# Kernel tuning notes

Measured on AMD Instinct MI355X. Metric: run time of the kernel, lower is better.

## Reference

```python
import jax, jax.numpy as jnp
import numpy as np

D = 1024  # in_features == latent_dim
EPS = 1e-5


def _layernorm(x, g, b):
    mu = jnp.mean(x, axis=-1, keepdims=True)
    var = jnp.mean(jnp.square(x - mu), axis=-1, keepdims=True)
    return (x - mu) * jax.lax.rsqrt(var + EPS) * g + b


def setup_inputs() -> dict:
    key = jax.random.key(0)
    ks = jax.random.split(key, 8)
    s = 1.0 / np.sqrt(D)
    return {
        "x": jax.random.normal(ks[0], (4, 4096, D), dtype=jnp.float32),
        "w_qkv": jax.random.uniform(ks[1], (3 * D, D), jnp.float32, -s, s),
        "w_o": jax.random.uniform(ks[2], (D, D), jnp.float32, -s, s),
        "w1": jax.random.uniform(ks[3], (D, D), jnp.float32, -s, s),
        "b1": jax.random.uniform(ks[4], (D,), jnp.float32, -s, s),
        "w2": jax.random.uniform(ks[5], (D, D), jnp.float32, -s, s),
        "b2": jax.random.uniform(ks[6], (D,), jnp.float32, -s, s),
        "ln1_g": jnp.ones((D,), jnp.float32),
        "ln1_b": jnp.zeros((D,), jnp.float32),
        "ln2_g": jnp.ones((D,), jnp.float32),
        "ln2_b": jnp.zeros((D,), jnp.float32),
    }


def reference(x, w_qkv, w_o, w1, b1, w2, b2, ln1_g, ln1_b, ln2_g, ln2_b):
    B, S, _ = x.shape
    scale = 1.0 / np.sqrt(D * 1)  # 1/sqrt(latent_dim * n_heads), n_heads=1
    qkv = jnp.einsum("bsd,ed->bse", x, w_qkv)            # [B,S,3D]
    qkv = qkv.reshape(B, S, 1, 3 * D).transpose(0, 2, 1, 3)  # [B,1,S,3D]
    q, k, v = jnp.split(qkv, 3, axis=-1)                  # each [B,1,S,D]
    logits = jnp.einsum("bhid,bhjd->bhij", q, k) * scale  # [B,1,S,S]
    # Faithful quirk: softmax over the HEAD axis (dim=1). With 1 head this
    # yields an all-ones attention matrix.
    attn = jax.nn.softmax(logits, axis=1)
    vals = jnp.einsum("bhij,bhjd->bhid", attn, v)         # [B,1,S,D]
    vals = vals.transpose(0, 2, 1, 3).reshape(B, S, D)
    attn_out = jnp.einsum("bsd,ed->bse", vals, w_o)
    # squeeze(-2) is a no-op for S>1
    x = _layernorm(x + attn_out, ln1_g, ln1_b)
    h = jax.nn.gelu(jnp.einsum("bsd,ed->bse", x, w1) + b1, approximate=False)
    mlp_out = jnp.einsum("bsd,ed->bse", h, w2) + b2
    return _layernorm(x + mlp_out, ln2_g, ln2_b)
```

## Files before the change

### kernel.cpp

```cpp
#include <hip/hip_runtime.h>
#include <hip/hip_bf16.h>

typedef __hip_bfloat16 bf16;
typedef __attribute__((ext_vector_type(8))) short short8;
typedef __attribute__((ext_vector_type(4))) float f32x4;

#define DDIM 1024
#define SEQ  4096
#define NB   4
#define MTOT (NB*SEQ)

static __device__ __forceinline__ unsigned short f2bf(float f) {
    __hip_bfloat16 h = __float2bfloat16(f);
    unsigned short u; __builtin_memcpy(&u, &h, 2); return u;
}
static __device__ __forceinline__ float bf2f(unsigned short u) {
    __hip_bfloat16 h; __builtin_memcpy(&h, &u, 2); return __bfloat162float(h);
}

__global__ __launch_bounds__(256) void prep_kernel(
    const float* __restrict__ w1, const float* __restrict__ w2,
    unsigned short* __restrict__ w1b, unsigned short* __restrict__ w2b,
    const float* __restrict__ x, float* __restrict__ partial)
{
    int bid = blockIdx.x;
    if (bid < 1024) {
        size_t idx = ((size_t)bid*256 + threadIdx.x) * 4;
        float4 a = *(const float4*)(w1 + idx);
        ushort4 o; o.x=f2bf(a.x); o.y=f2bf(a.y); o.z=f2bf(a.z); o.w=f2bf(a.w);
        *(ushort4*)(w1b + idx) = o;
        float4 b = *(const float4*)(w2 + idx);
        o.x=f2bf(b.x); o.y=f2bf(b.y); o.z=f2bf(b.z); o.w=f2bf(b.w);
        *(ushort4*)(w2b + idx) = o;
    } else {
        int idx = bid - 1024;
        int dx = idx & 3, b = (idx >> 2) & 3, sl = idx >> 4;
        int d  = dx*256 + threadIdx.x;
        const float* p = x + ((size_t)b*SEQ + (size_t)sl*128)*DDIM + d;
        float s = 0.f;
        #pragma unroll 4
        for (int i = 0; i < 128; ++i) s += p[(size_t)i*DDIM];
        partial[((size_t)sl*NB + b)*DDIM + d] = s;
    }
}

__global__ __launch_bounds__(256) void colsum_reduce_kernel(
    const float* __restrict__ partial, float* __restrict__ xsum)
{
    int d = blockIdx.x*256 + threadIdx.x;
    int b = blockIdx.y;
    float s = 0.f;
    #pragma unroll
    for (int sl = 0; sl < 32; ++sl) s += partial[((size_t)sl*NB + b)*DDIM + d];
    xsum[b*DDIM + d] = s;
}

__global__ __launch_bounds__(256) void matvec_kernel(
    const float* __restrict__ W, const float* __restrict__ vin, float* __restrict__ vout)
{
    int b = blockIdx.y;
    int g = threadIdx.x >> 4;
    int t = threadIdx.x & 15;
    int e = blockIdx.x*16 + g;
    const float* w = W + (size_t)e*DDIM;
    const float* v = vin + b*DDIM;
    float s = 0.f;
    for (int k = t; k < DDIM; k += 16) s += w[k]*v[k];
    #pragma unroll
    for (int o = 8; o; o >>= 1) s += __shfl_down(s, o, 16);
    if (t == 0) vout[b*DDIM + e] = s;
}

__global__ __launch_bounds__(256) void ln1_kernel(
    const float* __restrict__ x, const float* __restrict__ avec,
    const float* __restrict__ g1, const float* __restrict__ b1,
    unsigned short* __restrict__ x1b)
{
    int row = blockIdx.x;
    int b   = row >> 12;
    int tid = threadIdx.x;
    const float4* xr = (const float4*)(x + (size_t)row*DDIM);
    const float4* av = (const float4*)(avec + (size_t)b*DDIM);
    float4 xv = xr[tid], a4 = av[tid];
    float y0 = xv.x+a4.x, y1 = xv.y+a4.y, y2 = xv.z+a4.z, y3 = xv.w+a4.w;
    float s  = y0+y1+y2+y3;
    float ss = y0*y0+y1*y1+y2*y2+y3*y3;
    #pragma unroll
    for (int o = 32; o; o >>= 1) { s += __shfl_down(s,o,64); ss += __shfl_down(ss,o,64); }
    __shared__ float red[8];
    if ((tid&63) == 0) { red[tid>>6] = s; red[4+(tid>>6)] = ss; }
    __syncthreads();
    float St = red[0]+red[1]+red[2]+red[3];
    float Sq = red[4]+red[5]+red[6]+red[7];
    float mu = St*(1.0f/DDIM);
    float rs = rsqrtf(Sq*(1.0f/DDIM) - mu*mu + 1e-5f);
    float4 g4 = ((const float4*)g1)[tid];
    float4 bb = ((const float4*)b1)[tid];
    ushort4 o;
    o.x = f2bf((y0-mu)*rs*g4.x + bb.x);
    o.y = f2bf((y1-mu)*rs*g4.y + bb.y);
    o.z = f2bf((y2-mu)*rs*g4.z + bb.z);
    o.w = f2bf((y3-mu)*rs*g4.w + bb.w);
    *(ushort4*)(x1b + (size_t)row*DDIM + tid*4) = o;
}

__global__ __launch_bounds__(256, 2) void gemm1_kernel(
    const bf16* __restrict__ A, const bf16* __restrict__ Bw,
    const float* __restrict__ bias, unsigned short* __restrict__ outb)
{
    constexpr int K = 1024, N = 1024, BK = 64, NT = K / BK;
    __shared__ __align__(16) bf16 lds[2][2][128*BK];
    const int tid  = threadIdx.x;
    const int wave = tid >> 6, lane = tid & 63;

    int bid = blockIdx.x;
    int swz = (bid & 7) * 128 + (bid >> 3);
    const size_t bm = (size_t)(swz >> 3) * 128;
    const size_t bn = (size_t)(swz & 7) * 128;

    const int wm = wave >> 1;
    const int wn = wave & 1;

    const int srow = tid >> 3;
    const int skel = (((tid & 7) ^ ((tid >> 3) & 7)) << 3);

    const int fr = lane & 15;
    const int fs = lane >> 4;
    int foff[2];
    #pragma unroll
    for (int ks = 0; ks < 2; ++ks)
        foff[ks] = fr*128 + (((ks*4 + fs) ^ (fr & 7)) << 4);

    f32x4 acc[4][4] = {};
    const bf16* Ab = A  + bm * K;
    const bf16* Bb = Bw + bn * K;

    auto stage = [&](int b, int kt) {
        #pragma unroll
        for (int mat = 0; mat < 2; ++mat) {
            const bf16* src = (mat == 0 ? Ab : Bb);
            #pragma unroll
            for (int g = 0; g < 4; ++g) {
                int row = g*32 + srow;
                const bf16* gp = src + (size_t)row * K + kt*BK + skel;
                __builtin_amdgcn_global_load_lds(
                    (const __attribute__((address_space(1))) void*)gp,
                    (__attribute__((address_space(3))) void*)
                        ((char*)&lds[b][mat][0] + g*4096 + wave*1024),
                    16, 0, 0);
            }
        }
    };

    stage(0, 0);

    #pragma unroll 2
    for (int t = 0; t < NT; ++t) {
        const int cur = t & 1;
        if (t < NT-1) {
            stage(cur ^ 1, t + 1);
            asm volatile("s_waitcnt vmcnt(8)" ::: "memory");
        } else {
            asm volatile("s_waitcnt vmcnt(0)" ::: "memory");
        }
        __builtin_amdgcn_s_barrier();

        const char* LA = (const char*)&lds[cur][0][0] + wm*8192;
        const char* LB = (const char*)&lds[cur][1][0] + wn*8192;
        #pragma unroll
        for (int ks = 0; ks < 2; ++ks) {
            short8 af[4], bfr[4];
            #pragma unroll
            for (int m = 0; m < 4; ++m) af[m]  = *(const short8*)(LA + m*2048 + foff[ks]);
            #pragma unroll
            for (int n = 0; n < 4; ++n) bfr[n] = *(const short8*)(LB + n*2048 + foff[ks]);
            __builtin_amdgcn_s_setprio(1);
            #pragma unroll
            for (int m = 0; m < 4; ++m)
                #pragma unroll
                for (int n = 0; n < 4; ++n)
                    acc[m][n] = __builtin_amdgcn_mfma_f32_16x16x32_bf16(
                        af[m], bfr[n], acc[m][n], 0, 0, 0);
            __builtin_amdgcn_s_setprio(0);
        }
        __builtin_amdgcn_s_barrier();
    }

    #pragma unroll
    for (int n = 0; n < 4; ++n) {
        size_t col = bn + wn*64 + n*16 + fr;
        float bv = bias[col];
        #pragma unroll
        for (int m = 0; m < 4; ++m) {
            #pragma unroll
            for (int r = 0; r < 4; ++r) {
                size_t row = bm + wm*64 + m*16 + fs*4 + r;
                float v = acc[m][n][r] + bv;
                float ge = 0.5f*v*(1.0f + erff(v*0.70710678118f));
                outb[row*(size_t)N + col] = f2bf(ge);
            }
        }
    }
}

__global__ __launch_bounds__(256, 2) void gemm2_kernel(
    const bf16* __restrict__ A, const bf16* __restrict__ Bw,
    const float* __restrict__ bias, unsigned short* __restrict__ xy,
    float2* __restrict__ part)
{
    constexpr int K = 1024, N = 1024, BK = 64, NT = K / BK;
    __shared__ __align__(16) bf16 lds[2][2][128*BK];
    const int tid  = threadIdx.x;
    const int wave = tid >> 6, lane = tid & 63;

    int bid = blockIdx.x;
    int swz = (bid & 7) * 128 + (bid >> 3);
    const size_t bm = (size_t)(swz >> 3) * 128;
    const size_t bn = (size_t)(swz & 7) * 128;

    const int wm = wave >> 1;
    const int wn = wave & 1;

    const int srow = tid >> 3;
    const int skel = (((tid & 7) ^ ((tid >> 3) & 7)) << 3);

    const int fr = lane & 15;
    const int fs = lane >> 4;
    int foff[2];
    #pragma unroll
    for (int ks = 0; ks < 2; ++ks)
        foff[ks] = fr*128 + (((ks*4 + fs) ^ (fr & 7)) << 4);

    f32x4 acc[4][4] = {};
    const bf16* Ab = A  + bm * K;
    const bf16* Bb = Bw + bn * K;

    auto stage = [&](int b, int kt) {
        #pragma unroll
        for (int mat = 0; mat < 2; ++mat) {
            const bf16* src = (mat == 0 ? Ab : Bb);
            #pragma unroll
            for (int g = 0; g < 4; ++g) {
                int row = g*32 + srow;
                const bf16* gp = src + (size_t)row * K + kt*BK + skel;
                __builtin_amdgcn_global_load_lds(
                    (const __attribute__((address_space(1))) void*)gp,
                    (__attribute__((address_space(3))) void*)
                        ((char*)&lds[b][mat][0] + g*4096 + wave*1024),
                    16, 0, 0);
            }
        }
    };

    stage(0, 0);

    #pragma unroll 2
    for (int t = 0; t < NT; ++t) {
        const int cur = t & 1;
        if (t < NT-1) {
            stage(cur ^ 1, t + 1);
            asm volatile("s_waitcnt vmcnt(8)" ::: "memory");
        } else {
            asm volatile("s_waitcnt vmcnt(0)" ::: "memory");
        }
        __builtin_amdgcn_s_barrier();

        const char* LA = (const char*)&lds[cur][0][0] + wm*8192;
        const char* LB = (const char*)&lds[cur][1][0] + wn*8192;
        #pragma unroll
        for (int ks = 0; ks < 2; ++ks) {
            short8 af[4], bfr[4];
            #pragma unroll
            for (int m = 0; m < 4; ++m) af[m]  = *(const short8*)(LA + m*2048 + foff[ks]);
            #pragma unroll
            for (int n = 0; n < 4; ++n) bfr[n] = *(const short8*)(LB + n*2048 + foff[ks]);
            __builtin_amdgcn_s_setprio(1);
            #pragma unroll
            for (int m = 0; m < 4; ++m)
                #pragma unroll
                for (int n = 0; n < 4; ++n)
                    acc[m][n] = __builtin_amdgcn_mfma_f32_16x16x32_bf16(
                        af[m], bfr[n], acc[m][n], 0, 0, 0);
            __builtin_amdgcn_s_setprio(0);
        }
        __builtin_amdgcn_s_barrier();
    }

    float vs[4][4] = {}, vq[4][4] = {};
    #pragma unroll
    for (int n = 0; n < 4; ++n) {
        size_t col = bn + wn*64 + n*16 + fr;
        float bv = bias[col];
        #pragma unroll
        for (int m = 0; m < 4; ++m) {
            #pragma unroll
            for (int r = 0; r < 4; ++r) {
                size_t row = bm + wm*64 + m*16 + fs*4 + r;
                size_t idx = row*(size_t)N + col;
                float v = acc[m][n][r] + bv + bf2f(xy[idx]);
                unsigned short qb = f2bf(v);
                xy[idx] = qb;
                float vv = bf2f(qb);
                vs[m][r] += vv;
                vq[m][r] += vv*vv;
            }
        }
    }
    #pragma unroll
    for (int o = 1; o < 16; o <<= 1) {
        #pragma unroll
        for (int m = 0; m < 4; ++m)
            #pragma unroll
            for (int r = 0; r < 4; ++r) {
                vs[m][r] += __shfl_xor(vs[m][r], o);
                vq[m][r] += __shfl_xor(vq[m][r], o);
            }
    }
    float* lred = (float*)&lds[0][0][0];
    if (fr == 0) {
        #pragma unroll
        for (int m = 0; m < 4; ++m)
            #pragma unroll
            for (int r = 0; r < 4; ++r) {
                int rl = wm*64 + m*16 + fs*4 + r;
                lred[(wn*128 + rl)*2]     = vs[m][r];
                lred[(wn*128 + rl)*2 + 1] = vq[m][r];
            }
    }
    __syncthreads();
    if (tid < 128) {
        float s  = lred[tid*2]       + lred[(128 + tid)*2];
        float sq = lred[tid*2 + 1]   + lred[(128 + tid)*2 + 1];
        part[(bm + tid)*8 + (bn >> 7)] = make_float2(s, sq);
    }
}

__global__ __launch_bounds__(256) void ln2_apply_kernel(
    const unsigned short* __restrict__ yb, const float2* __restrict__ part,
    const float* __restrict__ g2, const float* __restrict__ b2,
    float* __restrict__ out)
{
    int row = blockIdx.x;
    int tid = threadIdx.x;
    float s = 0.f, sq = 0.f;
    #pragma unroll
    for (int i = 0; i < 8; ++i) {
        float2 p = part[(size_t)row*8 + i];
        s += p.x; sq += p.y;
    }
    float mu = s * (1.0f/DDIM);
    float rs = rsqrtf(sq * (1.0f/DDIM) - mu*mu + 1e-5f);
    ushort4 yv = *(const ushort4*)(yb + (size_t)row*DDIM + tid*4);
    float4 g4 = ((const float4*)g2)[tid];
    float4 bb = ((const float4*)b2)[tid];
    float4 o;
    o.x = (bf2f(yv.x) - mu)*rs*g4.x + bb.x;
    o.y = (bf2f(yv.y) - mu)*rs*g4.y + bb.y;
    o.z = (bf2f(yv.z) - mu)*rs*g4.z + bb.z;
    o.w = (bf2f(yv.w) - mu)*rs*g4.w + bb.w;
    ((float4*)(out + (size_t)row*DDIM))[tid] = o;
}

extern "C" void kernel_launch(void* const* d_in, const int* in_sizes, int n_in,
                              void* d_out, int out_size, void* d_ws, size_t ws_size,
                              hipStream_t stream)
{
    const float* x     = (const float*)d_in[0];
    const float* w_qkv = (const float*)d_in[1];
    const float* w_o   = (const float*)d_in[2];
    const float* w1    = (const float*)d_in[3];
    const float* b1    = (const float*)d_in[4];
    const float* w2    = (const float*)d_in[5];
    const float* b2    = (const float*)d_in[6];
    const float* ln1g  = (const float*)d_in[7];
    const float* ln1b  = (const float*)d_in[8];
    const float* ln2g  = (const float*)d_in[9];
    const float* ln2b  = (const float*)d_in[10];
    float* out = (float*)d_out;
    char* ws = (char*)d_ws;

    unsigned short* x1b = (unsigned short*)(ws);
    unsigned short* hb  = (unsigned short*)(ws + 33554432);
    unsigned short* w1b = (unsigned short*)(ws + 67108864);
    unsigned short* w2b = (unsigned short*)(ws + 69206016);
    float* partial = (float*)(ws + 71303168);
    float* xsum    = (float*)(ws + 71827456);
    float* tvec    = (float*)(ws + 71843840);
    float* avec    = (float*)(ws + 71860224);
    float2* lnpart = (float2*)(ws + 67108864);

    prep_kernel<<<dim3(1536), 256, 0, stream>>>(w1, w2, w1b, w2b, x, partial);
    colsum_reduce_kernel<<<dim3(4, NB), 256, 0, stream>>>(partial, xsum);
    matvec_kernel<<<dim3(64, NB), 256, 0, stream>>>(w_qkv + (size_t)2*DDIM*DDIM, xsum, tvec);
    matvec_kernel<<<dim3(64, NB), 256, 0, stream>>>(w_o, tvec, avec);
    ln1_kernel<<<dim3(MTOT), 256, 0, stream>>>(x, avec, ln1g, ln1b, x1b);
    gemm1_kernel<<<dim3(1024), 256, 0, stream>>>(
        (const bf16*)x1b, (const bf16*)w1b, b1, hb);
    gemm2_kernel<<<dim3(1024), 256, 0, stream>>>(
        (const bf16*)hb, (const bf16*)w2b, b2, x1b, lnpart);
    ln2_apply_kernel<<<dim3(MTOT), 256, 0, stream>>>(x1b, lnpart, ln2g, ln2b, out);
}
```

Measured before the change: 171.3 us.

## Fuse LN2 apply into gemm2 via last-block atomic counter; merge colsum into matvec

Removes the separate ln2_apply launch. Each gemm2 block bumps a per-row-block atomic counter, and the last of the 8 column blocks normalizes and writes the 128 output rows. The column-sum reduce kernel is also folded into the first matvec, which rebuilds the summed vector in LDS in every block. The trade-off is a serialized 128-row tail done by one block per row group, redundant partial-sum reads across the 64 matvec blocks, and a dependence on threadfence ordering for correctness.

```diff
diff --git a/kernel.cpp b/kernel.cpp
--- a/kernel.cpp
+++ b/kernel.cpp
@@ -21,9 +21,11 @@
 __global__ __launch_bounds__(256) void prep_kernel(
     const float* __restrict__ w1, const float* __restrict__ w2,
     unsigned short* __restrict__ w1b, unsigned short* __restrict__ w2b,
-    const float* __restrict__ x, float* __restrict__ partial)
+    const float* __restrict__ x, float* __restrict__ partial,
+    int* __restrict__ cnt)
 {
     int bid = blockIdx.x;
+    if (bid == 0 && threadIdx.x < 128) cnt[threadIdx.x] = 0;
     if (bid < 1024) {
         size_t idx = ((size_t)bid*256 + threadIdx.x) * 4;
         float4 a = *(const float4*)(w1 + idx);
@@ -44,15 +46,30 @@
     }
 }
 
-__global__ __launch_bounds__(256) void colsum_reduce_kernel(
-    const float* __restrict__ partial, float* __restrict__ xsum)
-{
-    int d = blockIdx.x*256 + threadIdx.x;
+__global__ __launch_bounds__(256) void matvec1_kernel(
+    const float* __restrict__ W, const float* __restrict__ partial,
+    float* __restrict__ vout)
+{
     int b = blockIdx.y;
+    __shared__ float vloc[DDIM];
+    #pragma unroll
+    for (int j = 0; j < 4; ++j) {
+        int d = j*256 + threadIdx.x;
+        float s = 0.f;
+        #pragma unroll
+        for (int sl = 0; sl < 32; ++sl) s += partial[((size_t)sl*NB + b)*DDIM + d];
+        vloc[d] = s;
+    }
+    __syncthreads();
+    int g = threadIdx.x >> 4;
+    int t = threadIdx.x & 15;
+    int e = blockIdx.x*16 + g;
+    const float* w = W + (size_t)e*DDIM;
     float s = 0.f;
-    #pragma unroll
-    for (int sl = 0; sl < 32; ++sl) s += partial[((size_t)sl*NB + b)*DDIM + d];
-    xsum[b*DDIM + d] = s;
+    for (int k = t; k < DDIM; k += 16) s += w[k]*vloc[k];
+    #pragma unroll
+    for (int o = 8; o; o >>= 1) s += __shfl_down(s, o, 16);
+    if (t == 0) vout[b*DDIM + e] = s;
 }
 
 __global__ __launch_bounds__(256) void matvec_kernel(
@@ -206,7 +223,9 @@
 __global__ __launch_bounds__(256, 2) void gemm2_kernel(
     const bf16* __restrict__ A, const bf16* __restrict__ Bw,
     const float* __restrict__ bias, unsigned short* __restrict__ xy,
-    float2* __restrict__ part)
+    float2* __restrict__ part, int* __restrict__ cnt,
+    const float* __restrict__ g2, const float* __restrict__ b2,
+    float* __restrict__ out)
 {
     constexpr int K = 1024, N = 1024, BK = 64, NT = K / BK;
     __shared__ __align__(16) bf16 lds[2][2][128*BK];
@@ -333,32 +352,37 @@
         float sq = lred[tid*2 + 1]   + lred[(128 + tid)*2 + 1];
         part[(bm + tid)*8 + (bn >> 7)] = make_float2(s, sq);
     }
-}
-
-__global__ __launch_bounds__(256) void ln2_apply_kernel(
-    const unsigned short* __restrict__ yb, const float2* __restrict__ part,
-    const float* __restrict__ g2, const float* __restrict__ b2,
-    float* __restrict__ out)
-{
-    int row = blockIdx.x;
-    int tid = threadIdx.x;
-    float s = 0.f, sq = 0.f;
-    #pragma unroll
-    for (int i = 0; i < 8; ++i) {
-        float2 p = part[(size_t)row*8 + i];
-        s += p.x; sq += p.y;
-    }
-    float mu = s * (1.0f/DDIM);
-    float rs = rsqrtf(sq * (1.0f/DDIM) - mu*mu + 1e-5f);
-    ushort4 yv = *(const ushort4*)(yb + (size_t)row*DDIM + tid*4);
-    float4 g4 = ((const float4*)g2)[tid];
-    float4 bb = ((const float4*)b2)[tid];
-    float4 o;
-    o.x = (bf2f(yv.x) - mu)*rs*g4.x + bb.x;
-    o.y = (bf2f(yv.y) - mu)*rs*g4.y + bb.y;
-    o.z = (bf2f(yv.z) - mu)*rs*g4.z + bb.z;
-    o.w = (bf2f(yv.w) - mu)*rs*g4.w + bb.w;
-    ((float4*)(out + (size_t)row*DDIM))[tid] = o;
+
+    __threadfence();
+    __shared__ int lastFlag;
+    if (tid == 0) {
+        int prev = atomicAdd(cnt + (int)(bm >> 7), 1);
+        lastFlag = (prev == 7);
+    }
+    __syncthreads();
+    if (lastFlag) {
+        __threadfence();
+        float4 g4 = ((const float4*)g2)[tid];
+        float4 bb = ((const float4*)b2)[tid];
+        for (int r = 0; r < 128; ++r) {
+            size_t row = bm + r;
+            float s = 0.f, sq = 0.f;
+            #pragma unroll
+            for (int i = 0; i < 8; ++i) {
+                float2 p = part[row*8 + i];
+                s += p.x; sq += p.y;
+            }
+            float mu = s * (1.0f/DDIM);
+            float rs = rsqrtf(sq * (1.0f/DDIM) - mu*mu + 1e-5f);
+            ushort4 yv = *(const ushort4*)(xy + row*DDIM + tid*4);
+            float4 o;
+            o.x = (bf2f(yv.x) - mu)*rs*g4.x + bb.x;
+            o.y = (bf2f(yv.y) - mu)*rs*g4.y + bb.y;
+            o.z = (bf2f(yv.z) - mu)*rs*g4.z + bb.z;
+            o.w = (bf2f(yv.w) - mu)*rs*g4.w + bb.w;
+            ((float4*)(out + row*DDIM))[tid] = o;
+        }
+    }
 }
 
 extern "C" void kernel_launch(void* const* d_in, const int* in_sizes, int n_in,
@@ -384,19 +408,18 @@
     unsigned short* w1b = (unsigned short*)(ws + 67108864);
     unsigned short* w2b = (unsigned short*)(ws + 69206016);
     float* partial = (float*)(ws + 71303168);
-    float* xsum    = (float*)(ws + 71827456);
     float* tvec    = (float*)(ws + 71843840);
     float* avec    = (float*)(ws + 71860224);
+    int*   cnt     = (int*)(ws + 71876608);
     float2* lnpart = (float2*)(ws + 67108864);
 
-    prep_kernel<<<dim3(1536), 256, 0, stream>>>(w1, w2, w1b, w2b, x, partial);
-    colsum_reduce_kernel<<<dim3(4, NB), 256, 0, stream>>>(partial, xsum);
-    matvec_kernel<<<dim3(64, NB), 256, 0, stream>>>(w_qkv + (size_t)2*DDIM*DDIM, xsum, tvec);
+    prep_kernel<<<dim3(1536), 256, 0, stream>>>(w1, w2, w1b, w2b, x, partial, cnt);
+    matvec1_kernel<<<dim3(64, NB), 256, 0, stream>>>(
+        w_qkv + (size_t)2*DDIM*DDIM, partial, tvec);
     matvec_kernel<<<dim3(64, NB), 256, 0, stream>>>(w_o, tvec, avec);
     ln1_kernel<<<dim3(MTOT), 256, 0, stream>>>(x, avec, ln1g, ln1b, x1b);
     gemm1_kernel<<<dim3(1024), 256, 0, stream>>>(
         (const bf16*)x1b, (const bf16*)w1b, b1, hb);
     gemm2_kernel<<<dim3(1024), 256, 0, stream>>>(
-        (const bf16*)hb, (const bf16*)w2b, b2, x1b, lnpart);
-    ln2_apply_kernel<<<dim3(MTOT), 256, 0, stream>>>(x1b, lnpart, ln2g, ln2b, out);
-}
+        (const bf16*)hb, (const bf16*)w2b, b2, x1b, lnpart, cnt, ln2g, ln2b, out);
+}
```

Result: slower. 366.1 us (+113.7%).
